# Kernel optimization log

Hardware: AMD Instinct MI355X
Metric: run time of the kernel (lower is better)

Reference implementation:

```python
import jax, jax.numpy as jnp
import numpy as np

N, E = 50000, 250000
SD, VM = 128, 64          # scalar channels, vector multiplicity (irreps: 128x0e + 64x1e)
EA, SH = 64, 4            # edge_attr dim, spherical-harmonics dim (1x0e + 1x1e)
H, FC = 16, 256
HD = FC // H              # head dim = 16
EPS = 1e-5


def _split(x):
    return x[:, :SD], x[:, SD:].reshape(-1, VM, 3)


def _ln(s, V):
    # equivariant layer norm: standardize scalars; RMS-normalize vector norms
    s = (s - s.mean(-1, keepdims=True)) * jax.lax.rsqrt(s.var(-1, keepdims=True) + EPS)
    vn = jax.lax.rsqrt(jnp.mean(jnp.sum(V * V, -1), -1, keepdims=True) + EPS)
    return s, V * vn[..., None]


def setup_inputs() -> dict:
    key = jax.random.key(0)
    ks = iter(jax.random.split(key, 48))
    rn = lambda shp, sc=1.0: jax.random.normal(next(ks), shp, dtype=jnp.float32) * sc
    w = lambda i, o: rn((i, o), 1.0 / np.sqrt(i))
    z = lambda d: jnp.zeros((d,), jnp.float32)
    return dict(
        node_features=rn((N, SD + 3 * VM)),
        edge_attr=rn((E, EA)),
        edge_sh=rn((E, SH)),
        Wq=w(SD, FC), bq=z(FC),
        Wk=w(SD, FC), bk=z(FC),
        We=w(EA, FC), be=z(FC),
        Wv_s=w(SD, SD), bv_s=z(SD), Wv_v=w(VM, VM),
        w_ss=w(SD, SD), w_vv_s=w(VM, SD), w_ssg=w(SD, VM), w_vvg=w(VM, VM),
        b_ms=z(SD), b_mg=z(VM),
        w_sv=w(SD, VM), w_vs=w(VM, VM), w_vvv=w(VM, VM),
        Wo_s=w(SD, SD), bo_s=z(SD), Wo_v=w(VM, VM),
        W1_s=w(SD, SD + VM), b1_s=z(SD + VM), W1_v=w(VM, VM),
        W2_s=w(SD, SD), b2_s=z(SD), W2_v=w(VM, VM),
        edge_index=jax.random.randint(next(ks), (2, E), 0, N, dtype=jnp.int32),
        batch=jnp.zeros((N,), jnp.int32),
    )


def reference(node_features, edge_attr, edge_sh, Wq, bq, Wk, bk, We, be,
              Wv_s, bv_s, Wv_v, w_ss, w_vv_s, w_ssg, w_vvg, b_ms, b_mg,
              w_sv, w_vs, w_vvv, Wo_s, bo_s, Wo_v,
              W1_s, b1_s, W1_v, W2_s, b2_s, W2_v, edge_index, batch):
    src, dst = edge_index[0], edge_index[1]
    ns, nV = _split(node_features)                        # [N,SD], [N,VM,3]

    # per-edge multi-head attention scores (gathered q/k + edge bias term)
    q = (ns[dst] @ Wq + bq).reshape(-1, H, HD)
    k = (ns[src] @ Wk + bk).reshape(-1, H, HD)
    ef = (edge_attr @ We + be).reshape(-1, H, HD)
    scores = ((q * k).sum(-1) + (q * ef).sum(-1)) / np.sqrt(HD)   # [E,H]

    # per-destination-node softmax (replaces the python unique(dst) loop)
    m = jax.ops.segment_max(scores, dst, num_segments=N)
    ex = jnp.exp(scores - m[dst])
    den = jax.ops.segment_sum(ex, dst, num_segments=N)
    attn = (ex / den[dst]).mean(-1, keepdims=True)                # [E,1]

    # v projection (o3.Linear) on source nodes
    vs = ns[src] @ Wv_s + bv_s                                    # [E,SD]
    Vv = jnp.einsum('evk,vu->euk', nV[src], Wv_v)                 # [E,VM,3]

    # message MLP: fully-connected tensor product with edge SH, norm, swish-gate
    shs, shv = edge_sh[:, 0], edge_sh[:, 1:4]
    s_in = vs * shs[:, None]                                      # 0e x 0e -> 0e
    dots = jnp.einsum('evk,ek->ev', Vv, shv)                      # 1e x 1e -> 0e
    ms = s_in @ w_ss + dots @ w_vv_s + b_ms                       # [E,SD] scalars
    mg = s_in @ w_ssg + dots @ w_vvg + b_mg                       # [E,VM] gates
    MV = ((vs @ w_sv)[:, :, None] * shv[:, None, :]               # 0e x 1e -> 1e
          + jnp.einsum('evk,vu->euk', Vv * shs[:, None, None], w_vs)   # 1e x 0e -> 1e
          + jnp.einsum('evk,vu->euk', jnp.cross(Vv, shv[:, None, :]), w_vvv))  # 1e x 1e -> 1e
    sg, MVn = _ln(jnp.concatenate([ms, mg], -1), MV)
    msg_s = jax.nn.silu(sg[:, :SD])
    msg_V = MVn * jax.nn.sigmoid(sg[:, SD:])[:, :, None]

    # attention-weighted scatter-sum aggregation to destination nodes
    agg_s = jax.ops.segment_sum(msg_s * attn, dst, num_segments=N)
    agg_V = jax.ops.segment_sum(msg_V * attn[:, :, None], dst, num_segments=N)

    # out projection + residual + norm1
    x_s = ns + (agg_s @ Wo_s + bo_s)
    x_V = nV + jnp.einsum('nvk,vu->nuk', agg_V, Wo_v)
    x_s, x_V = _ln(x_s, x_V)

    # gated equivariant FFN + residual + norm2
    f = x_s @ W1_s + b1_s                                         # [N,SD+VM]
    fV = jnp.einsum('nvk,vu->nuk', x_V, W1_v)
    gV = fV * jax.nn.sigmoid(f[:, SD:])[:, :, None]
    o_s = x_s + (jax.nn.silu(f[:, :SD]) @ W2_s + b2_s)
    o_V = x_V + jnp.einsum('nvk,vu->nuk', gV, W2_v)
    o_s, o_V = _ln(o_s, o_V)
    return jnp.concatenate([o_s, o_V.reshape(-1, 3 * VM)], -1)
```

## Files before the change

### kernel.cpp

```cpp
#include <hip/hip_runtime.h>
#include <hip/hip_bf16.h>

#define NNODE 50000
#define NEDGE 250000

typedef __hip_bfloat16 bf16;
typedef __attribute__((ext_vector_type(8))) short short8v;
typedef __attribute__((ext_vector_type(4))) float f32x4;

__device__ __forceinline__ float b2f(bf16 x){ return __bfloat162float(x); }
__device__ __forceinline__ bf16  f2b(float x){ return __float2bfloat16(x); }
__device__ __forceinline__ short f2s(float x){ bf16 h=f2b(x); short s; __builtin_memcpy(&s,&h,2); return s; }
__device__ __forceinline__ float s2f(short s){ bf16 h; __builtin_memcpy(&h,&s,2); return b2f(h); }
__device__ __forceinline__ float sigm(float x){ return 1.0f/(1.0f+__expf(-x)); }
__device__ __forceinline__ float wred64(float v){
  #pragma unroll
  for(int o=32;o>0;o>>=1) v+=__shfl_xor(v,o,64);
  return v;
}
__device__ __forceinline__ float gred16(float v){
  v+=__shfl_xor(v,1,64); v+=__shfl_xor(v,2,64); v+=__shfl_xor(v,4,64); v+=__shfl_xor(v,8,64);
  return v;
}
__device__ __forceinline__ int fragOff(int r, int k){
  int kt=k>>5, k32=k&31, half=k32>>4, g=(k32&15)>>2, j=k32&3;
  return (kt<<10)+((r+(g<<4))<<4)+(half<<3)+(j<<1);
}

#define T_WOS 0
#define T_WOV 32
#define T_W1S 40
#define T_W1V 88
#define T_W2S 96
#define T_W2V 128
#define T_WE  136
#define T_WQ  168
#define T_WK  232
#define T_WVS 296
#define T_WSS 328
#define T_WSSG 360
#define T_WSV 376
#define T_WVV 392
#define T_WVVS 400
#define T_WVVG 416
#define T_WVS2 424
#define T_WVVV 432
#define T_TOT 440

__global__ __launch_bounds__(64) void k_prep(
  const float* __restrict__ Wo_s, const float* __restrict__ Wo_v,
  const float* __restrict__ W1_s, const float* __restrict__ W1_v,
  const float* __restrict__ W2_s, const float* __restrict__ W2_v,
  const float* __restrict__ WeM,
  const float* __restrict__ Wq, const float* __restrict__ Wk,
  const float* __restrict__ Wv_s,
  const float* __restrict__ w_ss, const float* __restrict__ w_ssg,
  const float* __restrict__ w_sv,
  const float* __restrict__ Wv_v, const float* __restrict__ w_vv_s,
  const float* __restrict__ w_vvg, const float* __restrict__ w_vs,
  const float* __restrict__ w_vvv,
  short* __restrict__ P)
{
  const int T=blockIdx.x, l=threadIdx.x;
  const float* W; int N, KT, lt;
  if(T<T_WOV){ W=Wo_s; N=128; KT=4; lt=T; }
  else if(T<T_W1S){ W=Wo_v; N=64; KT=2; lt=T-T_WOV; }
  else if(T<T_W1V){ W=W1_s; N=192; KT=4; lt=T-T_W1S; }
  else if(T<T_W2S){ W=W1_v; N=64; KT=2; lt=T-T_W1V; }
  else if(T<T_W2V){ W=W2_s; N=128; KT=4; lt=T-T_W2S; }
  else if(T<T_WE){ W=W2_v; N=64; KT=2; lt=T-T_W2V; }
  else if(T<T_WQ){ W=WeM; N=256; KT=2; lt=T-T_WE; }
  else if(T<T_WK){ W=Wq; N=256; KT=4; lt=T-T_WQ; }
  else if(T<T_WVS){ W=Wk; N=256; KT=4; lt=T-T_WK; }
  else if(T<T_WSS){ W=Wv_s; N=128; KT=4; lt=T-T_WVS; }
  else if(T<T_WSSG){ W=w_ss; N=128; KT=4; lt=T-T_WSS; }
  else if(T<T_WSV){ W=w_ssg; N=64; KT=4; lt=T-T_WSSG; }
  else if(T<T_WVV){ W=w_sv; N=64; KT=4; lt=T-T_WSV; }
  else if(T<T_WVVS){ W=Wv_v; N=64; KT=2; lt=T-T_WVV; }
  else if(T<T_WVVG){ W=w_vv_s; N=128; KT=2; lt=T-T_WVVS; }
  else if(T<T_WVS2){ W=w_vvg; N=64; KT=2; lt=T-T_WVVG; }
  else if(T<T_WVVV){ W=w_vs; N=64; KT=2; lt=T-T_WVS2; }
  else { W=w_vvv; N=64; KT=2; lt=T-T_WVVV; }
  const int nt=lt/KT, kt=lt-nt*KT;
  const int col=nt*16+(l&15);
  short8v o;
  #pragma unroll
  for(int j=0;j<8;j++){
    int k=kt*32+((j>>2)<<4)+((l>>4)<<2)+(j&3);
    o[j]=f2s(W[(size_t)k*N+col]);
  }
  *(short8v*)(P+((size_t)T<<9)+(l<<3))=o;
}

__global__ __launch_bounds__(256) void k1_mfma(
  const float* __restrict__ nf, const short* __restrict__ P,
  const float* __restrict__ bq, const float* __restrict__ bk,
  const float* __restrict__ bvs,
  bf16* __restrict__ Q, bf16* __restrict__ K, bf16* __restrict__ NREC)
{
  __shared__ __align__(16) short nsF[4*512];
  __shared__ __align__(16) short vsF[4*512];
  const int t=threadIdx.x, l=t&63, w=t>>6;
  const int n0=blockIdx.x*16;
  for(int i=t;i<512;i+=256){
    int r=i>>5, c=(i&31)<<2;
    const float4 v=*(const float4*)&nf[(size_t)(n0+r)*320+c];
    short4 s; s.x=f2s(v.x); s.y=f2s(v.y); s.z=f2s(v.z); s.w=f2s(v.w);
    *(short4*)((char*)nsF+fragOff(r,c))=s;
  }
  __syncthreads();
  short8v a[4];
  #pragma unroll
  for(int kt=0;kt<4;kt++) a[kt]=*(const short8v*)((const char*)nsF+(kt<<10)+(l<<4));
  #pragma unroll
  for(int ii=0;ii<4;ii++){
    int nt=w+(ii<<2);
    f32x4 accq={0.f,0.f,0.f,0.f}, acck={0.f,0.f,0.f,0.f};
    #pragma unroll
    for(int kt=0;kt<4;kt++){
      short8v bq8=*(const short8v*)(P+(((size_t)(T_WQ+nt*4+kt))<<9)+(l<<3));
      short8v bk8=*(const short8v*)(P+(((size_t)(T_WK+nt*4+kt))<<9)+(l<<3));
      accq=__builtin_amdgcn_mfma_f32_16x16x32_bf16(a[kt],bq8,accq,0,0,0);
      acck=__builtin_amdgcn_mfma_f32_16x16x32_bf16(a[kt],bk8,acck,0,0,0);
    }
    int col=(nt<<4)+(l&15);
    float bqs=bq[col], bks=bk[col];
    #pragma unroll
    for(int r=0;r<4;r++){
      int row=((l>>4)<<2)+r;
      Q[(size_t)(n0+row)*256+col]=f2b(accq[r]+bqs);
      K[(size_t)(n0+row)*256+col]=f2b(acck[r]+bks);
    }
  }
  #pragma unroll
  for(int ii=0;ii<2;ii++){
    int nt=w+(ii<<2);
    f32x4 acc={0.f,0.f,0.f,0.f};
    #pragma unroll
    for(int kt=0;kt<4;kt++){
      short8v b=*(const short8v*)(P+(((size_t)(T_WVS+nt*4+kt))<<9)+(l<<3));
      acc=__builtin_amdgcn_mfma_f32_16x16x32_bf16(a[kt],b,acc,0,0,0);
    }
    int col=(nt<<4)+(l&15);
    float bv=bvs[col];
    #pragma unroll
    for(int r=0;r<4;r++){
      int row=((l>>4)<<2)+r;
      *(short*)((char*)vsF+fragOff(row,col))=f2s(acc[r]+bv);
    }
  }
  __syncthreads();
  #pragma unroll
  for(int kt=0;kt<4;kt++) a[kt]=*(const short8v*)((const char*)vsF+(kt<<10)+(l<<4));
  #pragma unroll
  for(int ii=0;ii<4;ii++){
    int nt=w+(ii<<2);
    int bt;
    if(nt<8) bt=T_WSS+nt*4;
    else if(nt<12) bt=T_WSSG+(nt-8)*4;
    else bt=T_WSV+(nt-12)*4;
    f32x4 acc={0.f,0.f,0.f,0.f};
    #pragma unroll
    for(int kt=0;kt<4;kt++){
      short8v b=*(const short8v*)(P+(((size_t)(bt+kt))<<9)+(l<<3));
      acc=__builtin_amdgcn_mfma_f32_16x16x32_bf16(a[kt],b,acc,0,0,0);
    }
    int col=(nt<<4)+(l&15);
    #pragma unroll
    for(int r=0;r<4;r++){
      int row=((l>>4)<<2)+r;
      NREC[(size_t)(n0+row)*1216+col]=f2b(acc[r]);
    }
  }
}

__global__ __launch_bounds__(256) void k2_mfma(
  const float* __restrict__ nf, const short* __restrict__ P,
  bf16* __restrict__ NREC)
{
  __shared__ __align__(16) short nvF[6*512];
  __shared__ __align__(16) short vvF[6*512];
  const int t=threadIdx.x, l=t&63, w=t>>6;
  const int n0=blockIdx.x*16;
  for(int i=t;i<3072;i+=256){
    int r=i/192, c=i-r*192;
    int v=c/3, k=c-3*v;
    float x=nf[(size_t)(n0+r)*320+128+c];
    *(short*)((char*)nvF+(k<<11)+fragOff(r,v))=f2s(x);
  }
  __syncthreads();
  #pragma unroll
  for(int jj=0;jj<3;jj++){
    int job=w+(jj<<2);
    int p=job>>2, nt=job&3;
    f32x4 acc={0.f,0.f,0.f,0.f};
    #pragma unroll
    for(int kt=0;kt<2;kt++){
      short8v a2=*(const short8v*)((const char*)nvF+(p<<11)+(kt<<10)+(l<<4));
      short8v b=*(const short8v*)(P+(((size_t)(T_WVV+nt*2+kt))<<9)+(l<<3));
      acc=__builtin_amdgcn_mfma_f32_16x16x32_bf16(a2,b,acc,0,0,0);
    }
    int col=(nt<<4)+(l&15);
    #pragma unroll
    for(int r=0;r<4;r++){
      int row=((l>>4)<<2)+r;
      *(short*)((char*)vvF+(p<<11)+fragOff(row,col))=f2s(acc[r]);
    }
  }
  __syncthreads();
  #pragma unroll
  for(int jj=0;jj<15;jj++){
    int job=w+(jj<<2);
    int p=job/20, r20=job-p*20;
    int nt, bt, off;
    if(r20<8){ nt=r20; bt=T_WVVS+nt*2; off=256+(p<<7); }
    else if(r20<12){ nt=r20-8; bt=T_WVVG+nt*2; off=640+(p<<6); }
    else if(r20<16){ nt=r20-12; bt=T_WVS2+nt*2; off=832+(p<<6); }
    else { nt=r20-16; bt=T_WVVV+nt*2; off=1024+(p<<6); }
    f32x4 acc={0.f,0.f,0.f,0.f};
    #pragma unroll
    for(int kt=0;kt<2;kt++){
      short8v a2=*(const short8v*)((const char*)vvF+(p<<11)+(kt<<10)+(l<<4));
      short8v b=*(const short8v*)(P+(((size_t)(bt+kt))<<9)+(l<<3));
      acc=__builtin_amdgcn_mfma_f32_16x16x32_bf16(a2,b,acc,0,0,0);
    }
    int col=(nt<<4)+(l&15);
    #pragma unroll
    for(int r=0;r<4;r++){
      int row=((l>>4)<<2)+r;
      NREC[(size_t)(n0+row)*1216+off+col]=f2b(acc[r]);
    }
  }
}

__global__ __launch_bounds__(256) void k_hist(const int* __restrict__ eidx, int* __restrict__ counts){
  int e=blockIdx.x*256+threadIdx.x;
  if(e<NEDGE) atomicAdd(&counts[eidx[NEDGE+e]],1);
}

__global__ __launch_bounds__(1024) void k_scan(const int* __restrict__ counts, int* __restrict__ off, int* __restrict__ cursor){
  __shared__ int wsum[16];
  __shared__ int woff[17];
  __shared__ int carry_s;
  const int t=threadIdx.x, ln=t&63, wid=t>>6;
  if(t==0) carry_s=0;
  __syncthreads();
  for(int base=0;base<NNODE;base+=1024){
    int idx=base+t;
    int v=(idx<NNODE)?counts[idx]:0;
    int incl=v;
    #pragma unroll
    for(int o=1;o<64;o<<=1){ int x=__shfl_up(incl,o,64); if(ln>=o) incl+=x; }
    if(ln==63) wsum[wid]=incl;
    __syncthreads();
    if(t<16){
      int s=wsum[t];
      #pragma unroll
      for(int o=1;o<16;o<<=1){ int x=__shfl_up(s,o,64); if(t>=o) s+=x; }
      woff[t+1]=s;
      if(t==0) woff[0]=0;
    }
    __syncthreads();
    int excl=carry_s+woff[wid]+(incl-v);
    if(idx<NNODE){ off[idx]=excl; cursor[idx]=excl; }
    __syncthreads();
    if(t==0) carry_s+=woff[16];
    __syncthreads();
  }
  if(t==0) off[NNODE]=NEDGE;
}

__global__ __launch_bounds__(256) void k_scatter(const int* __restrict__ eidx, int* __restrict__ cursor, int* __restrict__ eord){
  int e=blockIdx.x*256+threadIdx.x;
  if(e<NEDGE){
    int d=eidx[NEDGE+e];
    int pos=atomicAdd(&cursor[d],1);
    eord[pos]=e;
  }
}

__global__ __launch_bounds__(256) void k3_mfma(
  const float* __restrict__ eattr, const int* __restrict__ eidx,
  const short* __restrict__ P, const float* __restrict__ be,
  const bf16* __restrict__ Q, const bf16* __restrict__ K,
  float* __restrict__ SC)
{
  __shared__ __align__(16) short aeF[2*512];
  __shared__ __align__(16) float ef[16][260];
  __shared__ int ssrc[16], sdst[16];
  const int t=threadIdx.x, l=t&63, w=t>>6;
  const int e0=blockIdx.x*16;
  if(t<16){ ssrc[t]=eidx[e0+t]; sdst[t]=eidx[NEDGE+e0+t]; }
  {
    int r=t>>4, c4=(t&15)<<2;
    const float4 v=*(const float4*)&eattr[(size_t)(e0+r)*64+c4];
    short4 s; s.x=f2s(v.x); s.y=f2s(v.y); s.z=f2s(v.z); s.w=f2s(v.w);
    *(short4*)((char*)aeF+fragOff(r,c4))=s;
  }
  __syncthreads();
  {
    short8v a0=*(const short8v*)((const char*)aeF+(l<<4));
    short8v a1=*(const short8v*)((const char*)aeF+1024+(l<<4));
    #pragma unroll
    for(int ii=0;ii<4;ii++){
      int nt=w+(ii<<2);
      f32x4 acc={0.f,0.f,0.f,0.f};
      short8v b0=*(const short8v*)(P+(((size_t)(T_WE+nt*2+0))<<9)+(l<<3));
      short8v b1=*(const short8v*)(P+(((size_t)(T_WE+nt*2+1))<<9)+(l<<3));
      acc=__builtin_amdgcn_mfma_f32_16x16x32_bf16(a0,b0,acc,0,0,0);
      acc=__builtin_amdgcn_mfma_f32_16x16x32_bf16(a1,b1,acc,0,0,0);
      int col=(nt<<4)+(l&15);
      float bv=be[col];
      #pragma unroll
      for(int r=0;r<4;r++){ int row=((l>>4)<<2)+r; ef[row][col]=acc[r]+bv; }
    }
  }
  __syncthreads();
  {
    const int h=l&15, qt=l>>4;
    const int ch=h*16+(qt<<2);
    #pragma unroll
    for(int j=0;j<4;j++){
      int el=w*4+j;
      int s=ssrc[el], d=sdst[el];
      short4 qs=*(const short4*)((const short*)Q+(size_t)d*256+ch);
      short4 ks=*(const short4*)((const short*)K+(size_t)s*256+ch);
      const float4 e4=*(const float4*)&ef[el][ch];
      float p = s2f(qs.x)*(s2f(ks.x)+e4.x)
              + s2f(qs.y)*(s2f(ks.y)+e4.y)
              + s2f(qs.z)*(s2f(ks.z)+e4.z)
              + s2f(qs.w)*(s2f(ks.w)+e4.w);
      p += __shfl_xor(p,16,64);
      p += __shfl_xor(p,32,64);
      if(qt==0) SC[(size_t)(e0+el)*16+h]=p*0.25f;
    }
  }
}

__global__ __launch_bounds__(256) void k6_agg(
  const int* __restrict__ eidx, const float* __restrict__ esh,
  const bf16* __restrict__ NREC, const float* __restrict__ SC,
  const int* __restrict__ OFF, const int* __restrict__ EORD,
  const float* __restrict__ b_ms, const float* __restrict__ b_mg,
  float* __restrict__ AGS, float* __restrict__ AGV)
{
  const int l = threadIdx.x & 63;
  const int n = blockIdx.x*4 + (threadIdx.x>>6);
  const int beg=OFF[n], end=OFF[n+1];
  const float bmsa=b_ms[l], bmsb=b_ms[64+l], bmgv=b_mg[l];

  float mh=-1e30f;
  for(int i=beg;i<end;i++){
    int e=EORD[i];
    if(l<16) mh=fmaxf(mh, SC[(size_t)e*16+l]);
  }
  float dh=0.f;
  for(int i=beg;i<end;i++){
    int e=EORD[i];
    if(l<16) dh+=__expf(SC[(size_t)e*16+l]-mh);
  }
  float rdh = (end>beg && l<16) ? 1.f/dh : 0.f;

  float as0=0.f,as1=0.f,av0acc=0.f,av1acc=0.f,av2acc=0.f;
  for(int i=beg;i<end;i++){
    const int e=EORD[i];
    const int s=eidx[e];
    const float4 sh4=*(const float4*)&esh[(size_t)e*4];
    const float shs=sh4.x, sh0=sh4.y, sh1=sh4.z, sh2=sh4.w;
    float av=(l<16)? __expf(SC[(size_t)e*16+l]-mh)*rdh : 0.f;
    const float att=wred64(av)*(1.f/16.f);

    const bf16* R = NREC + (size_t)s*1216;
    const float s1a=b2f(R[l]),      s1b=b2f(R[64+l]);
    const float s2 =b2f(R[128+l]),  svv=b2f(R[192+l]);
    const float d1a0=b2f(R[256+l]),     d1a1=b2f(R[256+128+l]),  d1a2=b2f(R[256+256+l]);
    const float d1b0=b2f(R[256+64+l]),  d1b1=b2f(R[256+192+l]),  d1b2=b2f(R[256+320+l]);
    const float d20=b2f(R[640+l]),  d21=b2f(R[640+64+l]),  d22=b2f(R[640+128+l]);
    const float w0 =b2f(R[832+l]),  w1 =b2f(R[832+64+l]),  w2 =b2f(R[832+128+l]);
    const float c0 =b2f(R[1024+l]), c1 =b2f(R[1024+64+l]), c2 =b2f(R[1024+128+l]);

    float msa = shs*s1a + d1a0*sh0+d1a1*sh1+d1a2*sh2 + bmsa;
    float msb = shs*s1b + d1b0*sh0+d1b1*sh1+d1b2*sh2 + bmsb;
    float mgv = shs*s2  + d20*sh0 +d21*sh1 +d22*sh2  + bmgv;

    float sum = wred64(msa+msb+mgv);
    float sq  = wred64(msa*msa+msb*msb+mgv*mgv);
    float mean = sum*(1.f/192.f);
    float var  = sq*(1.f/192.f) - mean*mean;
    float rs   = rsqrtf(var + 1e-5f);

    float cr0 = c1*sh2 - c2*sh1;
    float cr1 = c2*sh0 - c0*sh2;
    float cr2 = c0*sh1 - c1*sh0;
    float mv0 = svv*sh0 + shs*w0 + cr0;
    float mv1 = svv*sh1 + shs*w1 + cr1;
    float mv2 = svv*sh2 + shs*w2 + cr2;
    float vsq = wred64(mv0*mv0+mv1*mv1+mv2*mv2);
    float vn  = rsqrtf(vsq*(1.f/64.f) + 1e-5f);

    float sga=(msa-mean)*rs, sgb=(msb-mean)*rs, sgg=(mgv-mean)*rs;
    float wV = vn * sigm(sgg) * att;
    as0 += sga*sigm(sga)*att;
    as1 += sgb*sigm(sgb)*att;
    av0acc += mv0*wV;
    av1acc += mv1*wV;
    av2acc += mv2*wV;
  }
  AGS[(size_t)n*128+l]     =as0;
  AGS[(size_t)n*128+64+l]  =as1;
  AGV[(size_t)n*192+l]     =av0acc;
  AGV[(size_t)n*192+64+l]  =av1acc;
  AGV[(size_t)n*192+128+l] =av2acc;
}

__global__ __launch_bounds__(256) void k7_mfma(
  const float* __restrict__ nf,
  const float* __restrict__ AGS, const float* __restrict__ AGV,
  const short* __restrict__ P,
  const float* __restrict__ bo_s, const float* __restrict__ b1_s, const float* __restrict__ b2_s,
  float* __restrict__ out)
{
  __shared__ float xs[16][132];
  __shared__ float xv[16][196];
  __shared__ float ff[16][196];
  __shared__ __align__(16) short asA[4*512];
  __shared__ __align__(16) short avA[6*512];
  __shared__ float smean[16], srs[16], svn[16];
  const int t=threadIdx.x, l=t&63, w=t>>6;
  const int n0=blockIdx.x*16;

  for(int i=t;i<2048;i+=256){ int r=i>>7,c=i&127; xs[r][c]=nf[(size_t)(n0+r)*320+c]; }
  for(int i=t;i<3072;i+=256){ int r=i/192,cc=i-r*192; int k=cc>>6,u=cc&63; xv[r][cc]=nf[(size_t)(n0+r)*320+128+u*3+k]; }
  for(int i=t;i<512;i+=256){
    int r=i>>5, c=(i&31)<<2;
    const float4 v=*(const float4*)&AGS[(size_t)(n0+r)*128+c];
    short4 s; s.x=f2s(v.x); s.y=f2s(v.y); s.z=f2s(v.z); s.w=f2s(v.w);
    *(short4*)((char*)asA+fragOff(r,c))=s;
  }
  for(int i=t;i<768;i+=256){
    int r=i/48, c=(i-r*48)<<2;
    const float4 v=*(const float4*)&AGV[(size_t)(n0+r)*192+c];
    int p=c>>6,u=c&63;
    short4 s; s.x=f2s(v.x); s.y=f2s(v.y); s.z=f2s(v.z); s.w=f2s(v.w);
    *(short4*)((char*)avA+(p<<11)+fragOff(r,u))=s;
  }
  __syncthreads();

  {
    short8v a[4];
    #pragma unroll
    for(int kt=0;kt<4;kt++) a[kt]=*(const short8v*)((const char*)asA+(kt<<10)+(l<<4));
    #pragma unroll
    for(int ii=0;ii<2;ii++){
      int nt=w+(ii<<2);
      f32x4 acc={0.f,0.f,0.f,0.f};
      #pragma unroll
      for(int kt=0;kt<4;kt++){
        short8v b=*(const short8v*)(P+(((size_t)(T_WOS+nt*4+kt))<<9)+(l<<3));
        acc=__builtin_amdgcn_mfma_f32_16x16x32_bf16(a[kt],b,acc,0,0,0);
      }
      int col=(nt<<4)+(l&15);
      float bv=bo_s[col];
      #pragma unroll
      for(int r=0;r<4;r++){ int row=((l>>4)<<2)+r; xs[row][col]+=acc[r]+bv; }
    }
    #pragma unroll
    for(int ii=0;ii<3;ii++){
      int tid=w*3+ii, p=tid>>2, nt2=tid&3;
      f32x4 acc={0.f,0.f,0.f,0.f};
      #pragma unroll
      for(int kt=0;kt<2;kt++){
        short8v a2=*(const short8v*)((const char*)avA+(((p<<1)+kt)<<10)+(l<<4));
        short8v b=*(const short8v*)(P+(((size_t)(T_WOV+nt2*2+kt))<<9)+(l<<3));
        acc=__builtin_amdgcn_mfma_f32_16x16x32_bf16(a2,b,acc,0,0,0);
      }
      int col=(p<<6)+(nt2<<4)+(l&15);
      #pragma unroll
      for(int r=0;r<4;r++){ int row=((l>>4)<<2)+r; xv[row][col]+=acc[r]; }
    }
  }
  __syncthreads();

  {
    const int nn=t>>4, g=t&15;
    float sum=0,sq=0;
    #pragma unroll
    for(int j=0;j<8;j++){ float x=xs[nn][g+16*j]; sum+=x; sq+=x*x; }
    sum=gred16(sum); sq=gred16(sq);
    float mean=sum*(1.f/128.f);
    float var=sq*(1.f/128.f)-mean*mean;
    float vsq=0;
    #pragma unroll
    for(int j=0;j<12;j++){ float x=xv[nn][g+16*j]; vsq+=x*x; }
    vsq=gred16(vsq);
    if(g==0){ smean[nn]=mean; srs[nn]=rsqrtf(var+1e-5f); svn[nn]=rsqrtf(vsq*(1.f/64.f)+1e-5f); }
  }
  __syncthreads();

  for(int i=t;i<512;i+=256){
    int r=i>>5, c=(i&31)<<2;
    float m=smean[r], rs=srs[r];
    float4 v=*(float4*)&xs[r][c];
    v.x=(v.x-m)*rs; v.y=(v.y-m)*rs; v.z=(v.z-m)*rs; v.w=(v.w-m)*rs;
    *(float4*)&xs[r][c]=v;
    short4 s; s.x=f2s(v.x); s.y=f2s(v.y); s.z=f2s(v.z); s.w=f2s(v.w);
    *(short4*)((char*)asA+fragOff(r,c))=s;
  }
  for(int i=t;i<768;i+=256){
    int r=i/48, c=(i-r*48)<<2;
    float vn=svn[r];
    float4 v=*(float4*)&xv[r][c];
    v.x*=vn; v.y*=vn; v.z*=vn; v.w*=vn;
    *(float4*)&xv[r][c]=v;
    int p=c>>6,u=c&63;
    short4 s; s.x=f2s(v.x); s.y=f2s(v.y); s.z=f2s(v.z); s.w=f2s(v.w);
    *(short4*)((char*)avA+(p<<11)+fragOff(r,u))=s;
  }
  __syncthreads();

  {
    short8v a[4];
    #pragma unroll
    for(int kt=0;kt<4;kt++) a[kt]=*(const short8v*)((const char*)asA+(kt<<10)+(l<<4));
    #pragma unroll
    for(int ii=0;ii<3;ii++){
      int nt=w+(ii<<2);
      f32x4 acc={0.f,0.f,0.f,0.f};
      #pragma unroll
      for(int kt=0;kt<4;kt++){
        short8v b=*(const short8v*)(P+(((size_t)(T_W1S+nt*4+kt))<<9)+(l<<3));
        acc=__builtin_amdgcn_mfma_f32_16x16x32_bf16(a[kt],b,acc,0,0,0);
      }
      int col=(nt<<4)+(l&15);
      float bv=b1_s[col];
      #pragma unroll
      for(int r=0;r<4;r++){ int row=((l>>4)<<2)+r; ff[row][col]=acc[r]+bv; }
    }
  }
  __syncthreads();

  f32x4 g4acc[3];
  {
    #pragma unroll
    for(int ii=0;ii<3;ii++){
      int tid=w*3+ii, p=tid>>2, nt2=tid&3;
      f32x4 acc={0.f,0.f,0.f,0.f};
      #pragma unroll
      for(int kt=0;kt<2;kt++){
        short8v a2=*(const short8v*)((const char*)avA+(((p<<1)+kt)<<10)+(l<<4));
        short8v b=*(const short8v*)(P+(((size_t)(T_W1V+nt2*2+kt))<<9)+(l<<3));
        acc=__builtin_amdgcn_mfma_f32_16x16x32_bf16(a2,b,acc,0,0,0);
      }
      g4acc[ii]=acc;
    }
    for(int i=t;i<512;i+=256){
      int r=i>>5, c=(i&31)<<2;
      float4 v=*(float4*)&ff[r][c];
      v.x=v.x*sigm(v.x); v.y=v.y*sigm(v.y); v.z=v.z*sigm(v.z); v.w=v.w*sigm(v.w);
      short4 s; s.x=f2s(v.x); s.y=f2s(v.y); s.z=f2s(v.z); s.w=f2s(v.w);
      *(short4*)((char*)asA+fragOff(r,c))=s;
    }
  }
  __syncthreads();

  {
    #pragma unroll
    for(int ii=0;ii<3;ii++){
      int tid=w*3+ii, p=tid>>2, nt2=tid&3;
      int uu=(nt2<<4)+(l&15);
      #pragma unroll
      for(int r=0;r<4;r++){
        int row=((l>>4)<<2)+r;
        float val=g4acc[ii][r]*sigm(ff[row][128+uu]);
        *(short*)((char*)avA+(p<<11)+fragOff(row,uu))=f2s(val);
      }
    }
  }
  __syncthreads();

  {
    short8v a[4];
    #pragma unroll
    for(int kt=0;kt<4;kt++) a[kt]=*(const short8v*)((const char*)asA+(kt<<10)+(l<<4));
    #pragma unroll
    for(int ii=0;ii<2;ii++){
      int nt=w+(ii<<2);
      f32x4 acc={0.f,0.f,0.f,0.f};
      #pragma unroll
      for(int kt=0;kt<4;kt++){
        short8v b=*(const short8v*)(P+(((size_t)(T_W2S+nt*4+kt))<<9)+(l<<3));
        acc=__builtin_amdgcn_mfma_f32_16x16x32_bf16(a[kt],b,acc,0,0,0);
      }
      int col=(nt<<4)+(l&15);
      float bv=b2_s[col];
      #pragma unroll
      for(int r=0;r<4;r++){ int row=((l>>4)<<2)+r; xs[row][col]+=acc[r]+bv; }
    }
    #pragma unroll
    for(int ii=0;ii<3;ii++){
      int tid=w*3+ii, p=tid>>2, nt2=tid&3;
      f32x4 acc={0.f,0.f,0.f,0.f};
      #pragma unroll
      for(int kt=0;kt<2;kt++){
        short8v a2=*(const short8v*)((const char*)avA+(((p<<1)+kt)<<10)+(l<<4));
        short8v b=*(const short8v*)(P+(((size_t)(T_W2V+nt2*2+kt))<<9)+(l<<3));
        acc=__builtin_amdgcn_mfma_f32_16x16x32_bf16(a2,b,acc,0,0,0);
      }
      int col=(p<<6)+(nt2<<4)+(l&15);
      #pragma unroll
      for(int r=0;r<4;r++){ int row=((l>>4)<<2)+r; xv[row][col]+=acc[r]; }
    }
  }
  __syncthreads();

  {
    const int nn=t>>4, g=t&15;
    float sum=0,sq=0;
    #pragma unroll
    for(int j=0;j<8;j++){ float x=xs[nn][g+16*j]; sum+=x; sq+=x*x; }
    sum=gred16(sum); sq=gred16(sq);
    float mean=sum*(1.f/128.f);
    float var=sq*(1.f/128.f)-mean*mean;
    float vsq=0;
    #pragma unroll
    for(int j=0;j<12;j++){ float x=xv[nn][g+16*j]; vsq+=x*x; }
    vsq=gred16(vsq);
    if(g==0){ smean[nn]=mean; srs[nn]=rsqrtf(var+1e-5f); svn[nn]=rsqrtf(vsq*(1.f/64.f)+1e-5f); }
  }
  __syncthreads();

  for(int i=t;i<16*320;i+=256){
    int nn=i/320, c=i-nn*320;
    float v;
    if(c<128) v=(xs[nn][c]-smean[nn])*srs[nn];
    else { int j=c-128; int u=j/3, k=j-u*3; v=xv[nn][(k<<6)+u]*svn[nn]; }
    out[(size_t)(n0+nn)*320+c]=v;
  }
}

extern "C" void kernel_launch(void* const* d_in, const int* in_sizes, int n_in,
                              void* d_out, int out_size, void* d_ws, size_t ws_size,
                              hipStream_t stream)
{
  (void)in_sizes; (void)n_in; (void)out_size; (void)ws_size;
  const float* nf    =(const float*)d_in[0];
  const float* eattr =(const float*)d_in[1];
  const float* esh   =(const float*)d_in[2];
  const float* Wq    =(const float*)d_in[3];  const float* bq  =(const float*)d_in[4];
  const float* Wk    =(const float*)d_in[5];  const float* bk  =(const float*)d_in[6];
  const float* We    =(const float*)d_in[7];  const float* be  =(const float*)d_in[8];
  const float* Wv_s  =(const float*)d_in[9];  const float* bv_s=(const float*)d_in[10];
  const float* Wv_v  =(const float*)d_in[11];
  const float* w_ss  =(const float*)d_in[12]; const float* w_vv_s=(const float*)d_in[13];
  const float* w_ssg =(const float*)d_in[14]; const float* w_vvg =(const float*)d_in[15];
  const float* b_ms  =(const float*)d_in[16]; const float* b_mg  =(const float*)d_in[17];
  const float* w_sv  =(const float*)d_in[18]; const float* w_vs  =(const float*)d_in[19];
  const float* w_vvv =(const float*)d_in[20];
  const float* Wo_s  =(const float*)d_in[21]; const float* bo_s  =(const float*)d_in[22];
  const float* Wo_v  =(const float*)d_in[23];
  const float* W1_s  =(const float*)d_in[24]; const float* b1_s  =(const float*)d_in[25];
  const float* W1_v  =(const float*)d_in[26];
  const float* W2_s  =(const float*)d_in[27]; const float* b2_s  =(const float*)d_in[28];
  const float* W2_v  =(const float*)d_in[29];
  const int*   eidx  =(const int*)d_in[30];
  float* out=(float*)d_out;

  char* w=(char*)d_ws;
  bf16* Q    =(bf16*)w;  w+=(size_t)NNODE*256*2;
  bf16* Kb   =(bf16*)w;  w+=(size_t)NNODE*256*2;
  bf16* NREC =(bf16*)w;  w+=(size_t)NNODE*1216*2;
  float* SC  =(float*)w; w+=(size_t)NEDGE*16*4;
  float* AGS =(float*)w; w+=(size_t)NNODE*128*4;
  float* AGV =(float*)w; w+=(size_t)NNODE*192*4;
  short* P   =(short*)w; w+=(size_t)T_TOT*512*2;
  int* COUNTS=(int*)w;   w+=(size_t)NNODE*4;
  int* OFFb  =(int*)w;   w+=(size_t)(NNODE+1)*4;
  int* CURSOR=(int*)w;   w+=(size_t)NNODE*4;
  int* EORDb =(int*)w;   w+=(size_t)NEDGE*4;

  hipMemsetAsync(COUNTS,0,(size_t)NNODE*4,stream);

  k_prep    <<<T_TOT,64,0,stream>>>(Wo_s,Wo_v,W1_s,W1_v,W2_s,W2_v,We,
                                    Wq,Wk,Wv_s,w_ss,w_ssg,w_sv,
                                    Wv_v,w_vv_s,w_vvg,w_vs,w_vvv,P);
  k_hist    <<<(NEDGE+255)/256,256,0,stream>>>(eidx,COUNTS);
  k_scan    <<<1,1024,0,stream>>>(COUNTS,OFFb,CURSOR);
  k_scatter <<<(NEDGE+255)/256,256,0,stream>>>(eidx,CURSOR,EORDb);
  k1_mfma   <<<NNODE/16,256,0,stream>>>(nf,P,bq,bk,bv_s,Q,Kb,NREC);
  k2_mfma   <<<NNODE/16,256,0,stream>>>(nf,P,NREC);
  k3_mfma   <<<NEDGE/16,256,0,stream>>>(eattr,eidx,P,be,Q,Kb,SC);
  k6_agg    <<<NNODE/4,256,0,stream>>>(eidx,esh,NREC,SC,OFFb,EORDb,b_ms,b_mg,AGS,AGV);
  k7_mfma   <<<NNODE/16,256,0,stream>>>(nf,AGS,AGV,P,bo_s,b1_s,b2_s,out);
}
```

Before: 523.8 us.

## Interleave per-node message record and precompute attention in separate kernel

The per-node record written by k1/k2 is re-laid out so that each lane's 20 needed bf16 values sit in five contiguous short4 groups (padded to 1280 per node). The aggregation kernel can then fetch them with five 8-byte loads instead of twenty scalar 2-byte loads. The softmax max/sum/normalise passes move from k6 into a new k5_att kernel that spreads edges across four 16-lane groups and writes one scalar attention weight per edge, which removes the serial per-edge exp and wave reduction from k6. In exchange there is an extra launch, an extra ATT buffer, and scattered narrow 2-byte stores in the producer kernels.

Measured after the change: 534.1 us. About the same (+2.0%).

```diff
diff --git a/kernel.cpp b/kernel.cpp
--- a/kernel.cpp
+++ b/kernel.cpp
@@ -92,11 +92,12 @@
   *(short8v*)(P+((size_t)T<<9)+(l<<3))=o;
 }
 
+
 __global__ __launch_bounds__(256) void k1_mfma(
   const float* __restrict__ nf, const short* __restrict__ P,
   const float* __restrict__ bq, const float* __restrict__ bk,
   const float* __restrict__ bvs,
-  bf16* __restrict__ Q, bf16* __restrict__ K, bf16* __restrict__ NREC)
+  bf16* __restrict__ Q, bf16* __restrict__ K, short* __restrict__ NREC2)
 {
   __shared__ __align__(16) short nsF[4*512];
   __shared__ __align__(16) short vsF[4*512];
@@ -166,17 +167,21 @@
       acc=__builtin_amdgcn_mfma_f32_16x16x32_bf16(a[kt],b,acc,0,0,0);
     }
     int col=(nt<<4)+(l&15);
+    int lane, sslot;
+    if(nt<8){ lane=col&63; sslot=(col>=64)?1:0; }
+    else if(nt<12){ lane=col-128; sslot=2; }
+    else { lane=col-192; sslot=3; }
     #pragma unroll
     for(int r=0;r<4;r++){
       int row=((l>>4)<<2)+r;
-      NREC[(size_t)(n0+row)*1216+col]=f2b(acc[r]);
+      NREC2[(size_t)(n0+row)*1280 + (lane<<2) + sslot]=f2s(acc[r]);
     }
   }
 }
 
 __global__ __launch_bounds__(256) void k2_mfma(
   const float* __restrict__ nf, const short* __restrict__ P,
-  bf16* __restrict__ NREC)
+  short* __restrict__ NREC2)
 {
   __shared__ __align__(16) short nvF[6*512];
   __shared__ __align__(16) short vvF[6*512];
@@ -212,11 +217,11 @@
   for(int jj=0;jj<15;jj++){
     int job=w+(jj<<2);
     int p=job/20, r20=job-p*20;
-    int nt, bt, off;
-    if(r20<8){ nt=r20; bt=T_WVVS+nt*2; off=256+(p<<7); }
-    else if(r20<12){ nt=r20-8; bt=T_WVVG+nt*2; off=640+(p<<6); }
-    else if(r20<16){ nt=r20-12; bt=T_WVS2+nt*2; off=832+(p<<6); }
-    else { nt=r20-16; bt=T_WVVV+nt*2; off=1024+(p<<6); }
+    int nt, bt, G0;
+    if(r20<8){ nt=r20; bt=T_WVVS+nt*2; G0=0; }
+    else if(r20<12){ nt=r20-8; bt=T_WVVG+nt*2; G0=1; }
+    else if(r20<16){ nt=r20-12; bt=T_WVS2+nt*2; G0=2; }
+    else { nt=r20-16; bt=T_WVVV+nt*2; G0=3; }
     f32x4 acc={0.f,0.f,0.f,0.f};
     #pragma unroll
     for(int kt=0;kt<2;kt++){
@@ -225,10 +230,17 @@
       acc=__builtin_amdgcn_mfma_f32_16x16x32_bf16(a2,b,acc,0,0,0);
     }
     int col=(nt<<4)+(l&15);
+    int G;
+    if(G0==0)      G = p*2 + (col>=64 ? 1 : 0);
+    else if(G0==1) G = 6 + p;
+    else if(G0==2) G = 9 + p;
+    else           G = 12 + p;
+    int lane = col & 63;
+    int addr = ((1+(G>>2))<<8) + (lane<<2) + (G&3);
     #pragma unroll
     for(int r=0;r<4;r++){
       int row=((l>>4)<<2)+r;
-      NREC[(size_t)(n0+row)*1216+off+col]=f2b(acc[r]);
+      NREC2[(size_t)(n0+row)*1280 + addr]=f2s(acc[r]);
     }
   }
 }
@@ -337,9 +349,35 @@
   }
 }
 
+__global__ __launch_bounds__(256) void k5_att(
+  const float* __restrict__ SC, const int* __restrict__ OFF,
+  const int* __restrict__ EORD, float* __restrict__ ATT)
+{
+  const int l=threadIdx.x&63;
+  const int n=blockIdx.x*4+(threadIdx.x>>6);
+  const int beg=OFF[n], end=OFF[n+1];
+  const int j=l>>4, h=l&15;
+  float mh=-1e30f;
+  for(int i=beg+j;i<end;i+=4) mh=fmaxf(mh, SC[(size_t)EORD[i]*16+h]);
+  mh=fmaxf(mh,__shfl_xor(mh,16,64));
+  mh=fmaxf(mh,__shfl_xor(mh,32,64));
+  float dh=0.f;
+  for(int i=beg+j;i<end;i+=4) dh+=__expf(SC[(size_t)EORD[i]*16+h]-mh);
+  dh+=__shfl_xor(dh,16,64);
+  dh+=__shfl_xor(dh,32,64);
+  float rdh=(end>beg)?1.f/dh:0.f;
+  for(int i0=beg;i0<end;i0+=4){
+    int i=i0+j;
+    int e=0; float a=0.f; bool act=(i<end);
+    if(act){ e=EORD[i]; a=__expf(SC[(size_t)e*16+h]-mh)*rdh; }
+    a=gred16(a);
+    if(h==0 && act) ATT[e]=a*(1.f/16.f);
+  }
+}
+
 __global__ __launch_bounds__(256) void k6_agg(
   const int* __restrict__ eidx, const float* __restrict__ esh,
-  const bf16* __restrict__ NREC, const float* __restrict__ SC,
+  const short* __restrict__ NREC2, const float* __restrict__ ATT,
   const int* __restrict__ OFF, const int* __restrict__ EORD,
   const float* __restrict__ b_ms, const float* __restrict__ b_mg,
   float* __restrict__ AGS, float* __restrict__ AGV)
@@ -349,39 +387,24 @@
   const int beg=OFF[n], end=OFF[n+1];
   const float bmsa=b_ms[l], bmsb=b_ms[64+l], bmgv=b_mg[l];
 
-  float mh=-1e30f;
-  for(int i=beg;i<end;i++){
-    int e=EORD[i];
-    if(l<16) mh=fmaxf(mh, SC[(size_t)e*16+l]);
-  }
-  float dh=0.f;
-  for(int i=beg;i<end;i++){
-    int e=EORD[i];
-    if(l<16) dh+=__expf(SC[(size_t)e*16+l]-mh);
-  }
-  float rdh = (end>beg && l<16) ? 1.f/dh : 0.f;
-
   float as0=0.f,as1=0.f,av0acc=0.f,av1acc=0.f,av2acc=0.f;
   for(int i=beg;i<end;i++){
     const int e=EORD[i];
     const int s=eidx[e];
+    const float att=ATT[e];
     const float4 sh4=*(const float4*)&esh[(size_t)e*4];
     const float shs=sh4.x, sh0=sh4.y, sh1=sh4.z, sh2=sh4.w;
-    float av=(l<16)? __expf(SC[(size_t)e*16+l]-mh)*rdh : 0.f;
-    const float att=wred64(av)*(1.f/16.f);
-
-    const bf16* R = NREC + (size_t)s*1216;
-    const float s1a=b2f(R[l]),      s1b=b2f(R[64+l]);
-    const float s2 =b2f(R[128+l]),  svv=b2f(R[192+l]);
-    const float d1a0=b2f(R[256+l]),     d1a1=b2f(R[256+128+l]),  d1a2=b2f(R[256+256+l]);
-    const float d1b0=b2f(R[256+64+l]),  d1b1=b2f(R[256+192+l]),  d1b2=b2f(R[256+320+l]);
-    const float d20=b2f(R[640+l]),  d21=b2f(R[640+64+l]),  d22=b2f(R[640+128+l]);
-    const float w0 =b2f(R[832+l]),  w1 =b2f(R[832+64+l]),  w2 =b2f(R[832+128+l]);
-    const float c0 =b2f(R[1024+l]), c1 =b2f(R[1024+64+l]), c2 =b2f(R[1024+128+l]);
-
-    float msa = shs*s1a + d1a0*sh0+d1a1*sh1+d1a2*sh2 + bmsa;
-    float msb = shs*s1b + d1b0*sh0+d1b1*sh1+d1b2*sh2 + bmsb;
-    float mgv = shs*s2  + d20*sh0 +d21*sh1 +d22*sh2  + bmgv;
+
+    const short* R = NREC2 + (size_t)s*1280 + (l<<2);
+    const short4 q0=*(const short4*)(R);
+    const short4 q1=*(const short4*)(R+256);
+    const short4 q2=*(const short4*)(R+512);
+    const short4 q3=*(const short4*)(R+768);
+    const short4 q4=*(const short4*)(R+1024);
+
+    float msa = shs*s2f(q0.x) + s2f(q1.x)*sh0 + s2f(q1.z)*sh1 + s2f(q2.x)*sh2 + bmsa;
+    float msb = shs*s2f(q0.y) + s2f(q1.y)*sh0 + s2f(q1.w)*sh1 + s2f(q2.y)*sh2 + bmsb;
+    float mgv = shs*s2f(q0.z) + s2f(q2.z)*sh0 + s2f(q2.w)*sh1 + s2f(q3.x)*sh2 + bmgv;
 
     float sum = wred64(msa+msb+mgv);
     float sq  = wred64(msa*msa+msb*msb+mgv*mgv);
@@ -389,6 +412,9 @@
     float var  = sq*(1.f/192.f) - mean*mean;
     float rs   = rsqrtf(var + 1e-5f);
 
+    const float svv=s2f(q0.w);
+    const float w0=s2f(q3.y), w1=s2f(q3.z), w2=s2f(q3.w);
+    const float c0=s2f(q4.x), c1=s2f(q4.y), c2=s2f(q4.z);
     float cr0 = c1*sh2 - c2*sh1;
     float cr1 = c2*sh0 - c0*sh2;
     float cr2 = c0*sh1 - c1*sh0;
@@ -668,8 +694,9 @@
   char* w=(char*)d_ws;
   bf16* Q    =(bf16*)w;  w+=(size_t)NNODE*256*2;
   bf16* Kb   =(bf16*)w;  w+=(size_t)NNODE*256*2;
-  bf16* NREC =(bf16*)w;  w+=(size_t)NNODE*1216*2;
+  short* NREC2=(short*)w; w+=(size_t)NNODE*1280*2;
   float* SC  =(float*)w; w+=(size_t)NEDGE*16*4;
+  float* ATT =(float*)w; w+=(size_t)NEDGE*4;
   float* AGS =(float*)w; w+=(size_t)NNODE*128*4;
   float* AGV =(float*)w; w+=(size_t)NNODE*192*4;
   short* P   =(short*)w; w+=(size_t)T_TOT*512*2;
@@ -686,9 +713,10 @@
   k_hist    <<<(NEDGE+255)/256,256,0,stream>>>(eidx,COUNTS);
   k_scan    <<<1,1024,0,stream>>>(COUNTS,OFFb,CURSOR);
   k_scatter <<<(NEDGE+255)/256,256,0,stream>>>(eidx,CURSOR,EORDb);
-  k1_mfma   <<<NNODE/16,256,0,stream>>>(nf,P,bq,bk,bv_s,Q,Kb,NREC);
-  k2_mfma   <<<NNODE/16,256,0,stream>>>(nf,P,NREC);
+  k1_mfma   <<<NNODE/16,256,0,stream>>>(nf,P,bq,bk,bv_s,Q,Kb,NREC2);
+  k2_mfma   <<<NNODE/16,256,0,stream>>>(nf,P,NREC2);
   k3_mfma   <<<NEDGE/16,256,0,stream>>>(eattr,eidx,P,be,Q,Kb,SC);
-  k6_agg    <<<NNODE/4,256,0,stream>>>(eidx,esh,NREC,SC,OFFb,EORDb,b_ms,b_mg,AGS,AGV);
+  k5_att    <<<NNODE/4,256,0,stream>>>(SC,OFFb,EORDb,ATT);
+  k6_agg    <<<NNODE/4,256,0,stream>>>(eidx,esh,NREC2,ATT,OFFb,EORDb,b_ms,b_mg,AGS,AGV);
   k7_mfma   <<<NNODE/16,256,0,stream>>>(nf,AGS,AGV,P,bo_s,b1_s,b2_s,out);
 }
```
